# Optimization experiments

Measured on AMD Instinct MI355X. Metric: run time of the kernel, lower is better.

The kernel has to match this reference:

```python
import jax, jax.numpy as jnp
import numpy as np

B, T, D, H = 64, 2048, 32, 256


def setup_inputs() -> dict:
    key = jax.random.key(0)
    ks = iter(jax.random.split(key, 20))
    def lin(k, fan_in, shape):
        return jax.random.normal(k, shape, dtype=jnp.float32) / np.sqrt(fan_in)
    return {
        "x":  jax.random.normal(next(ks), (B, T, D), dtype=jnp.float32),
        "W1": lin(next(ks), D, (D, H)),  "U1": lin(next(ks), H, (H, H)), "b1": jnp.zeros((H,), jnp.float32),
        "W2": lin(next(ks), H, (H, H)), "U2": lin(next(ks), H, (H, H)), "b2": jnp.zeros((H,), jnp.float32),
        "W3": lin(next(ks), H, (H, H)), "U3": lin(next(ks), H, (H, H)),
        "V3": lin(next(ks), H, (H, H)), "b3": jnp.zeros((H,), jnp.float32),
        "G1": lin(next(ks), 2 * H, (2 * H, H)), "bg1": jnp.zeros((H,), jnp.float32),
        "G2": lin(next(ks), 3 * H, (3 * H, H)), "bg2": jnp.zeros((H,), jnp.float32),
        "O1": lin(next(ks), H, (H, D)), "O2": lin(next(ks), H, (H, D)), "bo": jnp.zeros((D,), jnp.float32),
    }


def reference(x, W1, U1, b1, W2, U2, b2, W3, U3, V3, b3, G1, bg1, G2, bg2, O1, O2, bo):
    # x: [B, T, D]. Sequential gated residual RNN (hard_gate=False).
    Bn = x.shape[0]
    Hn = W1.shape[1]

    def step(carry, xt):
        h1, h2, h3, z1, z2 = carry
        h1 = jnp.tanh(xt @ W1 + h1 @ U1 + b1)
        h2 = z1 * jnp.tanh(h1 @ W2 + h2 @ U2 + b2) + (1.0 - z1) * h2
        h3 = z2 * jnp.tanh(h2 @ W3 + h3 @ U3 + h1 @ V3 + b3) + (1.0 - z2) * h3
        z1n = jax.nn.sigmoid(jnp.concatenate([h1, h2], axis=-1) @ G1 + bg1)
        z2n = jax.nn.sigmoid(jnp.concatenate([h1, h2, h3], axis=-1) @ G2 + bg2)
        z1 = z1n * z2n  # z1 <- z1 * z2 per original
        out = h2 @ O1 + h3 @ O2 + bo
        return (h1, h2, h3, z1, z2n), out

    h0 = jnp.zeros((Bn, Hn), x.dtype)
    z0 = jnp.ones((Bn, Hn), x.dtype)  # init gates = 1 (broadcast of ones(1,1))
    _, outs = jax.lax.scan(step, (h0, h0, h0, z0, z0), jnp.swapaxes(x, 0, 1))
    return jnp.swapaxes(outs, 0, 1)  # [B, T, D]
```

## Files before the change

### kernel.cpp

```cpp
#include <hip/hip_runtime.h>


#define T_LEN 2048
#define BATCH 64
#define DIM   32
#define HID   256
#define NRG   4
#define RING  32

typedef short    frag_ab __attribute__((ext_vector_type(8)));
typedef float    frag_cd __attribute__((ext_vector_type(4)));
typedef float    float4v __attribute__((ext_vector_type(4)));
typedef unsigned uint4v  __attribute__((ext_vector_type(4)));

#define MFMA16(a, b, c) __builtin_amdgcn_mfma_f32_16x16x32_bf16((a), (b), (c), 0, 0, 0)

#define S_W1 0
#define S_U1 1
#define S_W2 9
#define S_U2 17
#define S_W3 25
#define S_U3 33
#define S_V3 41
#define S_G1 49
#define S_G2 65
#define NSLOT 89
#define LDS_BYTES (NSLOT * 64 * 16)

#define H1_OFF   0
#define H1_SZ    (2 * BATCH * HID * 4)
#define H2R_OFF  (H1_OFF + H1_SZ)
#define H2R_SZ   (RING * BATCH * HID * 4)
#define H3R_OFF  (H2R_OFF + H2R_SZ)
#define H3R_SZ   (RING * BATCH * HID * 4)
#define CTL_OFF  (H3R_OFF + H3R_SZ)
#define CTL_SZ   (NRG * 16 * 4)

__device__ __forceinline__ unsigned short f2bf(float f) {
  unsigned u = __builtin_bit_cast(unsigned, f);
  u = (u + 0x7FFFu + ((u >> 16) & 1u)) >> 16;
  return (unsigned short)u;
}

__device__ __forceinline__ float fast_tanh(float x) {
  x = fminf(fmaxf(x, -15.f), 15.f);
  float e = __expf(2.f * x);
  return (e - 1.f) / (e + 1.f);
}

__device__ __forceinline__ float fast_sigmoid(float x) {
  x = fminf(fmaxf(x, -30.f), 30.f);
  return 1.f / (1.f + __expf(-x));
}

__device__ __forceinline__ void st_sys_u32(unsigned* p, unsigned v) {
  asm volatile("global_store_dword %0, %1, off sc0 sc1" :: "v"(p), "v"(v) : "memory");
}
__device__ __forceinline__ unsigned ld_sys_u32(const unsigned* p) {
  unsigned r;
  asm volatile("global_load_dword %0, %1, off sc0 sc1\n\t"
               "s_waitcnt vmcnt(0)"
               : "=v"(r) : "v"(p) : "memory");
  return r;
}

__device__ __forceinline__ void load16_sys(const unsigned* p, uint4v r[16]) {
  asm volatile(
      "global_load_dwordx4 %0, %16, off sc0 sc1\n\t"
      "global_load_dwordx4 %1, %16, off offset:16 sc0 sc1\n\t"
      "global_load_dwordx4 %2, %16, off offset:128 sc0 sc1\n\t"
      "global_load_dwordx4 %3, %16, off offset:144 sc0 sc1\n\t"
      "global_load_dwordx4 %4, %16, off offset:256 sc0 sc1\n\t"
      "global_load_dwordx4 %5, %16, off offset:272 sc0 sc1\n\t"
      "global_load_dwordx4 %6, %16, off offset:384 sc0 sc1\n\t"
      "global_load_dwordx4 %7, %16, off offset:400 sc0 sc1\n\t"
      "global_load_dwordx4 %8, %16, off offset:512 sc0 sc1\n\t"
      "global_load_dwordx4 %9, %16, off offset:528 sc0 sc1\n\t"
      "global_load_dwordx4 %10, %16, off offset:640 sc0 sc1\n\t"
      "global_load_dwordx4 %11, %16, off offset:656 sc0 sc1\n\t"
      "global_load_dwordx4 %12, %16, off offset:768 sc0 sc1\n\t"
      "global_load_dwordx4 %13, %16, off offset:784 sc0 sc1\n\t"
      "global_load_dwordx4 %14, %16, off offset:896 sc0 sc1\n\t"
      "global_load_dwordx4 %15, %16, off offset:912 sc0 sc1\n\t"
      "s_waitcnt vmcnt(0)"
      : "=v"(r[0]), "=v"(r[1]), "=v"(r[2]), "=v"(r[3]),
        "=v"(r[4]), "=v"(r[5]), "=v"(r[6]), "=v"(r[7]),
        "=v"(r[8]), "=v"(r[9]), "=v"(r[10]), "=v"(r[11]),
        "=v"(r[12]), "=v"(r[13]), "=v"(r[14]), "=v"(r[15])
      : "v"(p)
      : "memory");
}

__device__ __forceinline__ bool unpack_check(const uint4v r[16], unsigned tag16, frag_ab* a) {
  bool ok = true;
  #pragma unroll
  for (int kt = 0; kt < 8; ++kt) {
    #pragma unroll
    for (int j = 0; j < 8; ++j) {
      unsigned w = r[kt * 2 + (j >> 2)][j & 3];
      ok &= ((w >> 16) == tag16);
      a[kt][j] = (short)w;
    }
  }
  return ok;
}

__device__ __forceinline__ void read_state(const unsigned* p, unsigned proxy_off,
                                           unsigned tag16, frag_ab* a) {
  const unsigned* pp = p + proxy_off;
  while (!__all((ld_sys_u32(pp) >> 16) == tag16)) {}
  for (;;) {
    uint4v r[16];
    load16_sys(p, r);
    if (__all(unpack_check(r, tag16, a))) return;
  }
}

__device__ __forceinline__ void publish4(unsigned* pp, unsigned tag16, const float* v) {
  #pragma unroll
  for (int rr = 0; rr < 4; ++rr)
    st_sys_u32(pp + (size_t)rr * HID, (tag16 << 16) | (unsigned)f2bf(v[rr]));
}

__global__ void __launch_bounds__(64, 1)
resrnn_kernel(const float* __restrict__ x,
              const float* __restrict__ W1, const float* __restrict__ U1, const float* __restrict__ b1,
              const float* __restrict__ W2, const float* __restrict__ U2, const float* __restrict__ b2,
              const float* __restrict__ W3, const float* __restrict__ U3, const float* __restrict__ V3,
              const float* __restrict__ b3,
              const float* __restrict__ G1, const float* __restrict__ bg1,
              const float* __restrict__ G2, const float* __restrict__ bg2,
              const float* __restrict__ O1, const float* __restrict__ O2, const float* __restrict__ bo,
              float* __restrict__ out,
              unsigned* __restrict__ h1buf,
              unsigned* __restrict__ h2r,
              unsigned* __restrict__ h3r,
              unsigned* __restrict__ done)
{
  extern __shared__ char smem[];
  frag_ab* wf = (frag_ab*)smem;

  const int lane = (int)threadIdx.x;
  const int quad = lane >> 4;
  const int nn   = lane & 15;
  const int bid  = (int)blockIdx.x;

  const unsigned pxo = (unsigned)((nn & 7) * 32);

  if (bid < 64) {
    const int rg = bid & 3;
    const int sl = bid >> 2;
    const int colbase = sl * 16;

    {
      const float* mats[9] = { W1, U1, W2, U2, W3, U3, V3, G1, G2 };
      const int    nkt[9]  = { 1, 8, 8, 8, 8, 8, 8, 16, 24 };
      int slot = 0;
      for (int m = 0; m < 9; ++m) {
        const float* W = mats[m];
        for (int kt = 0; kt < nkt[m]; ++kt) {
          frag_ab f;
          #pragma unroll
          for (int j = 0; j < 8; ++j) {
            int k = kt * 32 + quad * 8 + j;
            f[j] = (short)f2bf(W[(size_t)k * HID + colbase + nn]);
          }
          wf[slot * 64 + lane] = f;
          ++slot;
        }
      }
    }

    const float b1l  = b1[colbase + nn];
    const float b2l  = b2[colbase + nn];
    const float b3l  = b3[colbase + nn];
    const float bg1l = bg1[colbase + nn];
    const float bg2l = bg2[colbase + nn];

    const frag_ab zf = {0,0,0,0,0,0,0,0};
    frag_ab a1n[8], a3old[8];
    #pragma unroll
    for (int i = 0; i < 8; ++i) { a1n[i] = zf; a3old[i] = zf; }
    float h2l[4] = {0.f,0.f,0.f,0.f};
    float h3l[4] = {0.f,0.f,0.f,0.f};
    float z1l[4] = {1.f,1.f,1.f,1.f};
    float z2l[4] = {1.f,1.f,1.f,1.f};

    const float*    xrow  = x + (size_t)(rg * 16 + nn) * T_LEN * DIM + quad * 8;
    unsigned*       h1pub = h1buf + ((size_t)(rg * 16 + quad * 4)) * HID + colbase + nn;
    const unsigned* h1rd  = h1buf + ((size_t)(rg * 16 + nn)) * HID + quad * 8;
    const size_t    h1st  = (size_t)BATCH * HID;

    {
      frag_cd p = {0.f,0.f,0.f,0.f};
      float4v xa = *(const float4v*)xrow;
      float4v xb = *(const float4v*)(xrow + 4);
      frag_ab xf;
      #pragma unroll
      for (int j = 0; j < 4; ++j) { xf[j] = (short)f2bf(xa[j]); xf[4 + j] = (short)f2bf(xb[j]); }
      p = MFMA16(xf, wf[S_W1 * 64 + lane], p);
      float v[4];
      #pragma unroll
      for (int rr = 0; rr < 4; ++rr) v[rr] = fast_tanh(p[rr] + b1l);
      publish4(h1pub, 1u, v);
    }
    read_state(h1rd, pxo, 1u, a1n);

    frag_cd p2a = {0.f,0.f,0.f,0.f}, p2b = {0.f,0.f,0.f,0.f};
    #pragma unroll
    for (int kt = 0; kt < 4; ++kt) p2a = MFMA16(a1n[kt], wf[(S_W2 + kt) * 64 + lane], p2a);
    #pragma unroll
    for (int kt = 4; kt < 8; ++kt) p2b = MFMA16(a1n[kt], wf[(S_W2 + kt) * 64 + lane], p2b);

    for (int t = 0; t < T_LEN; ++t) {
      const unsigned tag  = (unsigned)(t + 1);
      const int      slot = t & (RING - 1);

      if (t >= RING && (t & 7) == 0) {
        const unsigned need = (unsigned)(t - RING + 8);
        while (ld_sys_u32(done + rg * 16) < need) {}
      }

      #pragma unroll
      for (int rr = 0; rr < 4; ++rr) {
        float c = fast_tanh(p2a[rr] + p2b[rr] + b2l);
        h2l[rr] = z1l[rr] * c + (1.f - z1l[rr]) * h2l[rr];
      }
      publish4(h2r + ((size_t)slot * BATCH + rg * 16 + quad * 4) * HID + colbase + nn, tag, h2l);

      if (t + 1 < T_LEN) {
        frag_cd p = {0.f,0.f,0.f,0.f};
        const float* xp = xrow + (size_t)(t + 1) * DIM;
        float4v xa = *(const float4v*)xp;
        float4v xb = *(const float4v*)(xp + 4);
        frag_ab xf;
        #pragma unroll
        for (int j = 0; j < 4; ++j) { xf[j] = (short)f2bf(xa[j]); xf[4 + j] = (short)f2bf(xb[j]); }
        p = MFMA16(xf, wf[S_W1 * 64 + lane], p);
        #pragma unroll
        for (int kt = 0; kt < 8; ++kt) p = MFMA16(a1n[kt], wf[(S_U1 + kt) * 64 + lane], p);
        float v[4];
        #pragma unroll
        for (int rr = 0; rr < 4; ++rr) v[rr] = fast_tanh(p[rr] + b1l);
        publish4(h1pub + ((size_t)((t + 1) & 1)) * h1st, tag + 1u, v);
      }

      frag_cd p3u = {0.f,0.f,0.f,0.f}, pg1a = {0.f,0.f,0.f,0.f}, pg2a = {0.f,0.f,0.f,0.f};
      #pragma unroll
      for (int kt = 0; kt < 8; ++kt) p3u = MFMA16(a3old[kt], wf[(S_U3 + kt) * 64 + lane], p3u);
      #pragma unroll
      for (int kt = 0; kt < 8; ++kt) p3u = MFMA16(a1n[kt], wf[(S_V3 + kt) * 64 + lane], p3u);
      #pragma unroll
      for (int kt = 0; kt < 8; ++kt) pg1a = MFMA16(a1n[kt], wf[(S_G1 + kt) * 64 + lane], pg1a);
      #pragma unroll
      for (int kt = 0; kt < 8; ++kt) pg2a = MFMA16(a1n[kt], wf[(S_G2 + kt) * 64 + lane], pg2a);

      frag_ab a2[8];
      read_state(h2r + ((size_t)slot * BATCH + rg * 16 + nn) * HID + quad * 8, pxo, tag, a2);

      {
        frag_cd p3 = p3u;
        #pragma unroll
        for (int kt = 0; kt < 8; ++kt) p3 = MFMA16(a2[kt], wf[(S_W3 + kt) * 64 + lane], p3);
        #pragma unroll
        for (int rr = 0; rr < 4; ++rr) {
          float c = fast_tanh(p3[rr] + b3l);
          h3l[rr] = z2l[rr] * c + (1.f - z2l[rr]) * h3l[rr];
        }
        publish4(h3r + ((size_t)slot * BATCH + rg * 16 + quad * 4) * HID + colbase + nn, tag, h3l);
      }

      frag_cd pg1b = {0.f,0.f,0.f,0.f}, pg2b = {0.f,0.f,0.f,0.f};
      #pragma unroll
      for (int kt = 0; kt < 8; ++kt) pg1b = MFMA16(a2[kt], wf[(S_G1 + 8 + kt) * 64 + lane], pg1b);
      #pragma unroll
      for (int kt = 0; kt < 8; ++kt) pg2b = MFMA16(a2[kt], wf[(S_G2 + 8 + kt) * 64 + lane], pg2b);
      p2a = (frag_cd){0.f,0.f,0.f,0.f};
      p2b = (frag_cd){0.f,0.f,0.f,0.f};
      #pragma unroll
      for (int kt = 0; kt < 4; ++kt) p2a = MFMA16(a2[kt], wf[(S_U2 + kt) * 64 + lane], p2a);
      #pragma unroll
      for (int kt = 4; kt < 8; ++kt) p2b = MFMA16(a2[kt], wf[(S_U2 + kt) * 64 + lane], p2b);
      if (t + 1 < T_LEN) {
        read_state(h1rd + ((size_t)((t + 1) & 1)) * h1st, pxo, tag + 1u, a1n);
        #pragma unroll
        for (int kt = 0; kt < 4; ++kt) p2a = MFMA16(a1n[kt], wf[(S_W2 + kt) * 64 + lane], p2a);
        #pragma unroll
        for (int kt = 4; kt < 8; ++kt) p2b = MFMA16(a1n[kt], wf[(S_W2 + kt) * 64 + lane], p2b);
      }

      read_state(h3r + ((size_t)slot * BATCH + rg * 16 + nn) * HID + quad * 8, pxo, tag, a3old);

      frag_cd pg2c = {0.f,0.f,0.f,0.f};
      #pragma unroll
      for (int kt = 0; kt < 8; ++kt) pg2c = MFMA16(a3old[kt], wf[(S_G2 + 16 + kt) * 64 + lane], pg2c);
      #pragma unroll
      for (int rr = 0; rr < 4; ++rr) {
        float z1n = fast_sigmoid(pg1a[rr] + pg1b[rr] + bg1l);
        float z2n = fast_sigmoid(pg2a[rr] + pg2b[rr] + pg2c[rr] + bg2l);
        z1l[rr] = z1n * z2n;
        z2l[rr] = z2n;
      }
    }
  } else {
    const int rg = bid - 64;
    {
      const float* mats[2] = { O1, O2 };
      for (int m = 0; m < 2; ++m)
        for (int nt = 0; nt < 2; ++nt)
          for (int kt = 0; kt < 8; ++kt) {
            frag_ab f;
            #pragma unroll
            for (int j = 0; j < 8; ++j) {
              int k = kt * 32 + quad * 8 + j;
              f[j] = (short)f2bf(mats[m][(size_t)k * DIM + nt * 16 + nn]);
            }
            wf[(m * 16 + nt * 8 + kt) * 64 + lane] = f;
          }
    }
    const float bo0 = bo[nn];
    const float bo1 = bo[16 + nn];

    for (int t = 0; t < T_LEN; ++t) {
      const unsigned tag  = (unsigned)(t + 1);
      const int      slot = t & (RING - 1);
      const unsigned* g2p = h2r + ((size_t)slot * BATCH + rg * 16 + nn) * HID + quad * 8;
      const unsigned* g3p = h3r + ((size_t)slot * BATCH + rg * 16 + nn) * HID + quad * 8;

      while (!__all(((ld_sys_u32(g2p + pxo) >> 16) == tag) &
                    ((ld_sys_u32(g3p + pxo) >> 16) == tag))) {}

      frag_ab a2[8], a3[8];
      for (;;) {
        uint4v r2[16], r3[16];
        load16_sys(g2p, r2);
        load16_sys(g3p, r3);
        bool ok = unpack_check(r2, tag, a2);
        ok &= unpack_check(r3, tag, a3);
        if (__all(ok)) break;
      }

      frag_cd o0 = {0.f,0.f,0.f,0.f}, o1 = {0.f,0.f,0.f,0.f};
      #pragma unroll
      for (int kt = 0; kt < 8; ++kt) {
        o0 = MFMA16(a2[kt], wf[(0 * 16 + 0 * 8 + kt) * 64 + lane], o0);
        o1 = MFMA16(a2[kt], wf[(0 * 16 + 1 * 8 + kt) * 64 + lane], o1);
        o0 = MFMA16(a3[kt], wf[(1 * 16 + 0 * 8 + kt) * 64 + lane], o0);
        o1 = MFMA16(a3[kt], wf[(1 * 16 + 1 * 8 + kt) * 64 + lane], o1);
      }
      #pragma unroll
      for (int rr = 0; rr < 4; ++rr) {
        float* op = out + ((size_t)(rg * 16 + quad * 4 + rr) * T_LEN + t) * DIM;
        op[nn]      = o0[rr] + bo0;
        op[16 + nn] = o1[rr] + bo1;
      }
      if (lane == 0) st_sys_u32(done + rg * 16, tag);
    }
  }
}

extern "C" void kernel_launch(void* const* d_in, const int* in_sizes, int n_in,
                              void* d_out, int out_size, void* d_ws, size_t ws_size,
                              hipStream_t stream)
{
  (void)in_sizes; (void)n_in; (void)out_size; (void)ws_size;

  const float* x   = (const float*)d_in[0];
  const float* W1  = (const float*)d_in[1];
  const float* U1  = (const float*)d_in[2];
  const float* b1  = (const float*)d_in[3];
  const float* W2  = (const float*)d_in[4];
  const float* U2  = (const float*)d_in[5];
  const float* b2  = (const float*)d_in[6];
  const float* W3  = (const float*)d_in[7];
  const float* U3  = (const float*)d_in[8];
  const float* V3  = (const float*)d_in[9];
  const float* b3  = (const float*)d_in[10];
  const float* G1  = (const float*)d_in[11];
  const float* bg1 = (const float*)d_in[12];
  const float* G2  = (const float*)d_in[13];
  const float* bg2 = (const float*)d_in[14];
  const float* O1  = (const float*)d_in[15];
  const float* O2  = (const float*)d_in[16];
  const float* bo  = (const float*)d_in[17];

  char* ws = (char*)d_ws;
  unsigned* h1buf = (unsigned*)(ws + H1_OFF);
  unsigned* h2r   = (unsigned*)(ws + H2R_OFF);
  unsigned* h3r   = (unsigned*)(ws + H3R_OFF);
  unsigned* done  = (unsigned*)(ws + CTL_OFF);

  hipMemsetAsync(done, 0, CTL_SZ, stream);

  (void)hipFuncSetAttribute((const void*)resrnn_kernel,
                            hipFuncAttributeMaxDynamicSharedMemorySize, LDS_BYTES);

  resrnn_kernel<<<dim3(68), dim3(64), LDS_BYTES, stream>>>(
      x, W1, U1, b1, W2, U2, b2, W3, U3, V3, b3,
      G1, bg1, G2, bg2, O1, O2, bo,
      (float*)d_out, h1buf, h2r, h3r, done);
}
```

Baseline: 16.07 ms.

## Merge h1 exchange into h2 ring slot and batch state reads

Moves the next-step h1 publication into a second half of each h2 ring slot so h1 and h2 are read together with a single combined wait, removing the separate h1 read_state round trip per step. Drops the proxy-word spin polls in favour of directly retrying full tagged loads, and issues the two 16-load batches back-to-back with one waitcnt. The ring depth is halved to keep the buffer footprint similar. Risks: always publishing h1 (zeros at the final step) adds store traffic, and polling with full loads increases memory traffic while waiting.

```diff
diff --git a/kernel.cpp b/kernel.cpp
--- a/kernel.cpp
+++ b/kernel.cpp
@@ -6,7 +6,8 @@
 #define DIM   32
 #define HID   256
 #define NRG   4
-#define RING  32
+#define RING  16
+#define HALF  (BATCH * HID)
 
 typedef short    frag_ab __attribute__((ext_vector_type(8)));
 typedef float    frag_cd __attribute__((ext_vector_type(4)));
@@ -28,9 +29,9 @@
 #define LDS_BYTES (NSLOT * 64 * 16)
 
 #define H1_OFF   0
-#define H1_SZ    (2 * BATCH * HID * 4)
+#define H1_SZ    (BATCH * HID * 4)
 #define H2R_OFF  (H1_OFF + H1_SZ)
-#define H2R_SZ   (RING * BATCH * HID * 4)
+#define H2R_SZ   (RING * 2 * BATCH * HID * 4)
 #define H3R_OFF  (H2R_OFF + H2R_SZ)
 #define H3R_SZ   (RING * BATCH * HID * 4)
 #define CTL_OFF  (H3R_OFF + H3R_SZ)
@@ -64,31 +65,43 @@
   return r;
 }
 
+#define L16BODY                                                   \
+      "global_load_dwordx4 %0, %16, off sc0 sc1\n\t"              \
+      "global_load_dwordx4 %1, %16, off offset:16 sc0 sc1\n\t"    \
+      "global_load_dwordx4 %2, %16, off offset:128 sc0 sc1\n\t"   \
+      "global_load_dwordx4 %3, %16, off offset:144 sc0 sc1\n\t"   \
+      "global_load_dwordx4 %4, %16, off offset:256 sc0 sc1\n\t"   \
+      "global_load_dwordx4 %5, %16, off offset:272 sc0 sc1\n\t"   \
+      "global_load_dwordx4 %6, %16, off offset:384 sc0 sc1\n\t"   \
+      "global_load_dwordx4 %7, %16, off offset:400 sc0 sc1\n\t"   \
+      "global_load_dwordx4 %8, %16, off offset:512 sc0 sc1\n\t"   \
+      "global_load_dwordx4 %9, %16, off offset:528 sc0 sc1\n\t"   \
+      "global_load_dwordx4 %10, %16, off offset:640 sc0 sc1\n\t"  \
+      "global_load_dwordx4 %11, %16, off offset:656 sc0 sc1\n\t"  \
+      "global_load_dwordx4 %12, %16, off offset:768 sc0 sc1\n\t"  \
+      "global_load_dwordx4 %13, %16, off offset:784 sc0 sc1\n\t"  \
+      "global_load_dwordx4 %14, %16, off offset:896 sc0 sc1\n\t"  \
+      "global_load_dwordx4 %15, %16, off offset:912 sc0 sc1"
+
+#define L16OUTS                                                       \
+      : "=v"(r[0]), "=v"(r[1]), "=v"(r[2]), "=v"(r[3]),               \
+        "=v"(r[4]), "=v"(r[5]), "=v"(r[6]), "=v"(r[7]),               \
+        "=v"(r[8]), "=v"(r[9]), "=v"(r[10]), "=v"(r[11]),             \
+        "=v"(r[12]), "=v"(r[13]), "=v"(r[14]), "=v"(r[15])            \
+      : "v"(p)                                                        \
+      : "memory"
+
 __device__ __forceinline__ void load16_sys(const unsigned* p, uint4v r[16]) {
-  asm volatile(
-      "global_load_dwordx4 %0, %16, off sc0 sc1\n\t"
-      "global_load_dwordx4 %1, %16, off offset:16 sc0 sc1\n\t"
-      "global_load_dwordx4 %2, %16, off offset:128 sc0 sc1\n\t"
-      "global_load_dwordx4 %3, %16, off offset:144 sc0 sc1\n\t"
-      "global_load_dwordx4 %4, %16, off offset:256 sc0 sc1\n\t"
-      "global_load_dwordx4 %5, %16, off offset:272 sc0 sc1\n\t"
-      "global_load_dwordx4 %6, %16, off offset:384 sc0 sc1\n\t"
-      "global_load_dwordx4 %7, %16, off offset:400 sc0 sc1\n\t"
-      "global_load_dwordx4 %8, %16, off offset:512 sc0 sc1\n\t"
-      "global_load_dwordx4 %9, %16, off offset:528 sc0 sc1\n\t"
-      "global_load_dwordx4 %10, %16, off offset:640 sc0 sc1\n\t"
-      "global_load_dwordx4 %11, %16, off offset:656 sc0 sc1\n\t"
-      "global_load_dwordx4 %12, %16, off offset:768 sc0 sc1\n\t"
-      "global_load_dwordx4 %13, %16, off offset:784 sc0 sc1\n\t"
-      "global_load_dwordx4 %14, %16, off offset:896 sc0 sc1\n\t"
-      "global_load_dwordx4 %15, %16, off offset:912 sc0 sc1\n\t"
-      "s_waitcnt vmcnt(0)"
-      : "=v"(r[0]), "=v"(r[1]), "=v"(r[2]), "=v"(r[3]),
-        "=v"(r[4]), "=v"(r[5]), "=v"(r[6]), "=v"(r[7]),
-        "=v"(r[8]), "=v"(r[9]), "=v"(r[10]), "=v"(r[11]),
-        "=v"(r[12]), "=v"(r[13]), "=v"(r[14]), "=v"(r[15])
-      : "v"(p)
-      : "memory");
+  asm volatile(L16BODY "\n\ts_waitcnt vmcnt(0)" L16OUTS);
+}
+__device__ __forceinline__ void load16_nw(const unsigned* p, uint4v r[16]) {
+  asm volatile(L16BODY L16OUTS);
+}
+__device__ __forceinline__ void order16(uint4v r[16]) {
+  asm volatile("" : "+v"(r[0]), "+v"(r[1]), "+v"(r[2]), "+v"(r[3]),
+                    "+v"(r[4]), "+v"(r[5]), "+v"(r[6]), "+v"(r[7]) :: "memory");
+  asm volatile("" : "+v"(r[8]), "+v"(r[9]), "+v"(r[10]), "+v"(r[11]),
+                    "+v"(r[12]), "+v"(r[13]), "+v"(r[14]), "+v"(r[15]) :: "memory");
 }
 
 __device__ __forceinline__ bool unpack_check(const uint4v r[16], unsigned tag16, frag_ab* a) {
@@ -105,14 +118,28 @@
   return ok;
 }
 
-__device__ __forceinline__ void read_state(const unsigned* p, unsigned proxy_off,
-                                           unsigned tag16, frag_ab* a) {
-  const unsigned* pp = p + proxy_off;
-  while (!__all((ld_sys_u32(pp) >> 16) == tag16)) {}
+__device__ __forceinline__ void read_state(const unsigned* p, unsigned tag16, frag_ab* a) {
   for (;;) {
     uint4v r[16];
     load16_sys(p, r);
     if (__all(unpack_check(r, tag16, a))) return;
+  }
+}
+
+__device__ __forceinline__ void read_state2(const unsigned* p2, const unsigned* p1,
+                                            unsigned tag16, frag_ab* a2, frag_ab* a1) {
+  for (;;) {
+    uint4v r1[16], r2[16];
+    {
+      uint4v* r = r1; const unsigned* p = p1; load16_nw(p, r);
+    }
+    {
+      uint4v* r = r2; const unsigned* p = p2; load16_sys(p, r);
+    }
+    order16(r1);
+    bool ok = unpack_check(r2, tag16, a2);
+    ok &= unpack_check(r1, tag16, a1);
+    if (__all(ok)) return;
   }
 }
 
@@ -145,8 +172,6 @@
   const int nn   = lane & 15;
   const int bid  = (int)blockIdx.x;
 
-  const unsigned pxo = (unsigned)((nn & 7) * 32);
-
   if (bid < 64) {
     const int rg = bid & 3;
     const int sl = bid >> 2;
@@ -186,10 +211,9 @@
     float z1l[4] = {1.f,1.f,1.f,1.f};
     float z2l[4] = {1.f,1.f,1.f,1.f};
 
-    const float*    xrow  = x + (size_t)(rg * 16 + nn) * T_LEN * DIM + quad * 8;
-    unsigned*       h1pub = h1buf + ((size_t)(rg * 16 + quad * 4)) * HID + colbase + nn;
-    const unsigned* h1rd  = h1buf + ((size_t)(rg * 16 + nn)) * HID + quad * 8;
-    const size_t    h1st  = (size_t)BATCH * HID;
+    const float* xrow = x + (size_t)(rg * 16 + nn) * T_LEN * DIM + quad * 8;
+    const size_t puboff = ((size_t)(rg * 16 + quad * 4)) * HID + colbase + nn;
+    const size_t rdoff  = ((size_t)(rg * 16 + nn)) * HID + quad * 8;
 
     {
       frag_cd p = {0.f,0.f,0.f,0.f};
@@ -202,9 +226,9 @@
       float v[4];
       #pragma unroll
       for (int rr = 0; rr < 4; ++rr) v[rr] = fast_tanh(p[rr] + b1l);
-      publish4(h1pub, 1u, v);
-    }
-    read_state(h1rd, pxo, 1u, a1n);
+      publish4(h1buf + puboff, 1u, v);
+    }
+    read_state(h1buf + rdoff, 1u, a1n);
 
     frag_cd p2a = {0.f,0.f,0.f,0.f}, p2b = {0.f,0.f,0.f,0.f};
     #pragma unroll
@@ -215,6 +239,7 @@
     for (int t = 0; t < T_LEN; ++t) {
       const unsigned tag  = (unsigned)(t + 1);
       const int      slot = t & (RING - 1);
+      unsigned* h2slot = h2r + (size_t)slot * (2 * HALF);
 
       if (t >= RING && (t & 7) == 0) {
         const unsigned need = (unsigned)(t - RING + 8);
@@ -226,23 +251,25 @@
         float c = fast_tanh(p2a[rr] + p2b[rr] + b2l);
         h2l[rr] = z1l[rr] * c + (1.f - z1l[rr]) * h2l[rr];
       }
-      publish4(h2r + ((size_t)slot * BATCH + rg * 16 + quad * 4) * HID + colbase + nn, tag, h2l);
-
-      if (t + 1 < T_LEN) {
-        frag_cd p = {0.f,0.f,0.f,0.f};
-        const float* xp = xrow + (size_t)(t + 1) * DIM;
-        float4v xa = *(const float4v*)xp;
-        float4v xb = *(const float4v*)(xp + 4);
-        frag_ab xf;
-        #pragma unroll
-        for (int j = 0; j < 4; ++j) { xf[j] = (short)f2bf(xa[j]); xf[4 + j] = (short)f2bf(xb[j]); }
-        p = MFMA16(xf, wf[S_W1 * 64 + lane], p);
-        #pragma unroll
-        for (int kt = 0; kt < 8; ++kt) p = MFMA16(a1n[kt], wf[(S_U1 + kt) * 64 + lane], p);
-        float v[4];
-        #pragma unroll
-        for (int rr = 0; rr < 4; ++rr) v[rr] = fast_tanh(p[rr] + b1l);
-        publish4(h1pub + ((size_t)((t + 1) & 1)) * h1st, tag + 1u, v);
+      publish4(h2slot + puboff, tag, h2l);
+
+      {
+        float v[4] = {0.f, 0.f, 0.f, 0.f};
+        if (t + 1 < T_LEN) {
+          frag_cd p = {0.f,0.f,0.f,0.f};
+          const float* xp = xrow + (size_t)(t + 1) * DIM;
+          float4v xa = *(const float4v*)xp;
+          float4v xb = *(const float4v*)(xp + 4);
+          frag_ab xf;
+          #pragma unroll
+          for (int j = 0; j < 4; ++j) { xf[j] = (short)f2bf(xa[j]); xf[4 + j] = (short)f2bf(xb[j]); }
+          p = MFMA16(xf, wf[S_W1 * 64 + lane], p);
+          #pragma unroll
+          for (int kt = 0; kt < 8; ++kt) p = MFMA16(a1n[kt], wf[(S_U1 + kt) * 64 + lane], p);
+          #pragma unroll
+          for (int rr = 0; rr < 4; ++rr) v[rr] = fast_tanh(p[rr] + b1l);
+        }
+        publish4(h2slot + HALF + puboff, tag, v);
       }
 
       frag_cd p3u = {0.f,0.f,0.f,0.f}, pg1a = {0.f,0.f,0.f,0.f}, pg2a = {0.f,0.f,0.f,0.f};
@@ -256,7 +283,7 @@
       for (int kt = 0; kt < 8; ++kt) pg2a = MFMA16(a1n[kt], wf[(S_G2 + kt) * 64 + lane], pg2a);
 
       frag_ab a2[8];
-      read_state(h2r + ((size_t)slot * BATCH + rg * 16 + nn) * HID + quad * 8, pxo, tag, a2);
+      read_state2(h2slot + rdoff, h2slot + HALF + rdoff, tag, a2, a1n);
 
       {
         frag_cd p3 = p3u;
@@ -267,7 +294,7 @@
           float c = fast_tanh(p3[rr] + b3l);
           h3l[rr] = z2l[rr] * c + (1.f - z2l[rr]) * h3l[rr];
         }
-        publish4(h3r + ((size_t)slot * BATCH + rg * 16 + quad * 4) * HID + colbase + nn, tag, h3l);
+        publish4(h3r + (size_t)slot * HALF + puboff, tag, h3l);
       }
 
       frag_cd pg1b = {0.f,0.f,0.f,0.f}, pg2b = {0.f,0.f,0.f,0.f};
@@ -282,14 +309,13 @@
       #pragma unroll
       for (int kt = 4; kt < 8; ++kt) p2b = MFMA16(a2[kt], wf[(S_U2 + kt) * 64 + lane], p2b);
       if (t + 1 < T_LEN) {
-        read_state(h1rd + ((size_t)((t + 1) & 1)) * h1st, pxo, tag + 1u, a1n);
         #pragma unroll
         for (int kt = 0; kt < 4; ++kt) p2a = MFMA16(a1n[kt], wf[(S_W2 + kt) * 64 + lane], p2a);
         #pragma unroll
         for (int kt = 4; kt < 8; ++kt) p2b = MFMA16(a1n[kt], wf[(S_W2 + kt) * 64 + lane], p2b);
       }
 
-      read_state(h3r + ((size_t)slot * BATCH + rg * 16 + nn) * HID + quad * 8, pxo, tag, a3old);
+      read_state(h3r + (size_t)slot * HALF + rdoff, tag, a3old);
 
       frag_cd pg2c = {0.f,0.f,0.f,0.f};
       #pragma unroll
@@ -320,21 +346,24 @@
     }
     const float bo0 = bo[nn];
     const float bo1 = bo[16 + nn];
+    const size_t rdoff = ((size_t)(rg * 16 + nn)) * HID + quad * 8;
 
     for (int t = 0; t < T_LEN; ++t) {
       const unsigned tag  = (unsigned)(t + 1);
       const int      slot = t & (RING - 1);
-      const unsigned* g2p = h2r + ((size_t)slot * BATCH + rg * 16 + nn) * HID + quad * 8;
-      const unsigned* g3p = h3r + ((size_t)slot * BATCH + rg * 16 + nn) * HID + quad * 8;
-
-      while (!__all(((ld_sys_u32(g2p + pxo) >> 16) == tag) &
-                    ((ld_sys_u32(g3p + pxo) >> 16) == tag))) {}
+      const unsigned* g2p = h2r + (size_t)slot * (2 * HALF) + rdoff;
+      const unsigned* g3p = h3r + (size_t)slot * HALF + rdoff;
 
       frag_ab a2[8], a3[8];
       for (;;) {
         uint4v r2[16], r3[16];
-        load16_sys(g2p, r2);
-        load16_sys(g3p, r3);
+        {
+          uint4v* r = r2; const unsigned* p = g2p; load16_nw(p, r);
+        }
+        {
+          uint4v* r = r3; const unsigned* p = g3p; load16_sys(p, r);
+        }
+        order16(r2);
         bool ok = unpack_check(r2, tag, a2);
         ok &= unpack_check(r3, tag, a3);
         if (__all(ok)) break;
```

Result: no change. 15.78 ms (-1.8%).
